# Kernel optimization log

Hardware: AMD Instinct MI355X
Metric: run time of the kernel (lower is better)

The kernel has to match this reference:

```python
import jax, jax.numpy as jnp
import numpy as np


def setup_inputs() -> dict:
    key = jax.random.key(0)
    k1, k2, k3, k4 = jax.random.split(key, 4)
    B, S, IN, H = 4, 2048, 512, 1024
    x = jax.random.normal(k1, (B, S, IN), dtype=jnp.float32)
    W1 = jax.random.normal(k2, (IN, H), dtype=jnp.float32) * (1.0 / np.sqrt(IN))
    b1 = jax.random.normal(k3, (H,), dtype=jnp.float32) * 0.02
    Wq = jax.random.normal(k4, (H, H), dtype=jnp.float32) * (1.0 / np.sqrt(H))
    return {"x": x, "W1": W1, "b1": b1, "Wq": Wq, "atten_size": 16}


def reference(x, W1, b1, Wq, atten_size):
    A = atten_size
    B, S, _ = x.shape
    H = W1.shape[1]
    h = jax.nn.relu(jnp.einsum('bsi,ih->bsh', x, W1) + b1)  # [B,S,H]
    # zero-pad sequence dim by A on each side
    padded = jnp.pad(h, ((0, 0), (A, A), (0, 0)))  # [B,S+2A,H]
    # torch: stack(roll(padded, k, 1) for k in -A..A, dim=2) then slice [A:-A]
    # => x_nei[b, i, j] = padded[b, 2A + i - j]
    idx = 2 * A + jnp.arange(S)[:, None] - jnp.arange(2 * A + 1)[None, :]  # [S,W]
    x_nei = padded[:, idx, :]  # [B,S,W,H]
    q = jnp.einsum('bsh,hk->bsk', h, Wq)  # [B,S,H]
    scores = jnp.einsum('bsh,bswh->bsw', q, x_nei) / jnp.sqrt(jnp.asarray(H, x.dtype))
    w = jax.nn.softmax(scores, axis=2)  # softmax over window axis
    out = jnp.einsum('bsw,bswh->bsh', w, x_nei)
    return out
```

## Files before the change

### kernel.cpp

```cpp
#include <hip/hip_runtime.h>
#include <stdint.h>

constexpr int BATCH = 4;
constexpr int SEQ   = 2048;
constexpr int DIN   = 512;
constexpr int DH    = 1024;
constexpr int BS    = BATCH * SEQ;
constexpr int AP    = 32;
constexpr int AW    = 64;

typedef float  floatx4 __attribute__((ext_vector_type(4)));
typedef short  bf16x8  __attribute__((ext_vector_type(8)));

static __device__ __forceinline__ unsigned short f2bf(float f) {
  union { float f; unsigned u; } v; v.f = f;
  unsigned r = (v.u + 0x7fffu + ((v.u >> 16) & 1u)) >> 16;
  return (unsigned short)r;
}

static __device__ __forceinline__ void gld_lds16(const unsigned short* g, const short* l) {
  typedef const __attribute__((address_space(1))) void* gvp;
  typedef __attribute__((address_space(3))) void* lvp;
  __builtin_amdgcn_global_load_lds((gvp)(uintptr_t)g, (lvp)(unsigned)(uintptr_t)l, 16, 0, 0);
}

__global__ __launch_bounds__(256) void convert_x_k(const float* __restrict__ X,
                                                   unsigned short* __restrict__ Xb) {
  const int t = blockIdx.x * 256 + threadIdx.x;
  const float4 a = ((const float4*)X)[(size_t)t * 2];
  const float4 b = ((const float4*)X)[(size_t)t * 2 + 1];
  __align__(16) unsigned short o[8];
  o[0] = f2bf(a.x); o[1] = f2bf(a.y); o[2] = f2bf(a.z); o[3] = f2bf(a.w);
  o[4] = f2bf(b.x); o[5] = f2bf(b.y); o[6] = f2bf(b.z); o[7] = f2bf(b.w);
  *(uint4*)(Xb + (size_t)t * 8) = *(const uint4*)o;
}

__global__ __launch_bounds__(256) void transpose_w_k(const float* __restrict__ W1,
                                                     const float* __restrict__ Wq,
                                                     unsigned short* __restrict__ w1t,
                                                     unsigned short* __restrict__ wqt) {
  __shared__ float t[32][33];
  const bool isW1 = blockIdx.y < 16;
  const float* in = isW1 ? W1 : Wq;
  unsigned short* out = isW1 ? w1t : wqt;
  const int R = isW1 ? DIN : DH;
  const int C = DH;
  const int r0 = (isW1 ? blockIdx.y : (blockIdx.y - 16)) * 32;
  const int c0 = blockIdx.x * 32;
  const int tx = threadIdx.x & 31, ty = threadIdx.x >> 5;
  for (int i = ty; i < 32; i += 8) t[i][tx] = in[(size_t)(r0 + i) * C + c0 + tx];
  __syncthreads();
  for (int i = ty; i < 32; i += 8) out[(size_t)(c0 + i) * R + r0 + tx] = f2bf(t[tx][i]);
}

__global__ __launch_bounds__(256) void gemm1_k(const unsigned short* __restrict__ Ab,
                                               const unsigned short* __restrict__ Bt,
                                               const float* __restrict__ bias,
                                               unsigned short* __restrict__ outB,
                                               unsigned short* __restrict__ outBT) {
  const int M = BS, N = DH, K = DIN;
  __shared__ __align__(16) short As0[128 * 32], As1[128 * 32];
  __shared__ __align__(16) short Bs0[128 * 32], Bs1[128 * 32];
  const int tid  = threadIdx.x;
  const int m0   = blockIdx.x * 128, n0 = blockIdx.y * 128;
  const int wv   = tid >> 6, lane = tid & 63;
  const int wm   = (wv >> 1) * 64, wn = (wv & 1) * 64;
  const int l16  = lane & 15, quad = lane >> 4;

  const int ra = lane >> 2, ca = (lane & 3) * 8;
  const unsigned short* gA = Ab + (size_t)(m0 + wv * 32 + ra) * K + ca;
  const unsigned short* gB = Bt + (size_t)(n0 + wv * 32 + ra) * K + ca;
  const short* lA0a = &As0[wv * 1024];
  const short* lA0b = &As0[wv * 1024 + 512];
  const short* lA1a = &As1[wv * 1024];
  const short* lA1b = &As1[wv * 1024 + 512];
  const short* lB0a = &Bs0[wv * 1024];
  const short* lB0b = &Bs0[wv * 1024 + 512];
  const short* lB1a = &Bs1[wv * 1024];
  const short* lB1b = &Bs1[wv * 1024 + 512];

  floatx4 acc[4][4];
  for (int i = 0; i < 4; i++)
    for (int j = 0; j < 4; j++) acc[i][j] = {0.f, 0.f, 0.f, 0.f};

  for (int ks = 0; ks < K / 64; ++ks) {
    __syncthreads();
    gld_lds16(gA, lA0a); gld_lds16(gA + 16 * K, lA0b);
    gld_lds16(gA + 32, lA1a); gld_lds16(gA + 16 * K + 32, lA1b);
    gld_lds16(gB, lB0a); gld_lds16(gB + 16 * K, lB0b);
    gld_lds16(gB + 32, lB1a); gld_lds16(gB + 16 * K + 32, lB1b);
    gA += 64; gB += 64;
    __syncthreads();
    bf16x8 af[4], bfr[4];
    for (int i = 0; i < 4; i++)
      af[i] = *(const bf16x8*)&As0[(wm + i * 16 + l16) * 32 + quad * 8];
    for (int j = 0; j < 4; j++)
      bfr[j] = *(const bf16x8*)&Bs0[(wn + j * 16 + l16) * 32 + quad * 8];
    for (int i = 0; i < 4; i++)
      for (int j = 0; j < 4; j++)
        acc[i][j] = __builtin_amdgcn_mfma_f32_16x16x32_bf16(af[i], bfr[j], acc[i][j], 0, 0, 0);
    for (int i = 0; i < 4; i++)
      af[i] = *(const bf16x8*)&As1[(wm + i * 16 + l16) * 32 + quad * 8];
    for (int j = 0; j < 4; j++)
      bfr[j] = *(const bf16x8*)&Bs1[(wn + j * 16 + l16) * 32 + quad * 8];
    for (int i = 0; i < 4; i++)
      for (int j = 0; j < 4; j++)
        acc[i][j] = __builtin_amdgcn_mfma_f32_16x16x32_bf16(af[i], bfr[j], acc[i][j], 0, 0, 0);
  }

  for (int j = 0; j < 4; j++) {
    const int col = n0 + wn + j * 16 + l16;
    const float bv = bias[col];
    for (int i = 0; i < 4; i++) {
      const int rowb = m0 + wm + i * 16 + quad * 4;
      float v[4];
      for (int r = 0; r < 4; r++) v[r] = fmaxf(acc[i][j][r] + bv, 0.f);
      for (int r = 0; r < 4; r++) outB[(size_t)(rowb + r) * N + col] = f2bf(v[r]);
      ushort4 o4; o4.x = f2bf(v[0]); o4.y = f2bf(v[1]); o4.z = f2bf(v[2]); o4.w = f2bf(v[3]);
      *(ushort4*)(outBT + (size_t)col * M + rowb) = o4;
    }
  }
}

__global__ __launch_bounds__(256) void gemm2_k(const unsigned short* __restrict__ Ab,
                                               const unsigned short* __restrict__ Bt,
                                               unsigned short* __restrict__ outB) {
  const int N = DH, K = DH;
  __shared__ __align__(16) short As0[128 * 32], As1[128 * 32];
  __shared__ __align__(16) short Bs0[128 * 32], Bs1[128 * 32];
  const int tid  = threadIdx.x;
  const int m0   = blockIdx.x * 128, n0 = blockIdx.y * 128;
  const int wv   = tid >> 6, lane = tid & 63;
  const int wm   = (wv >> 1) * 64, wn = (wv & 1) * 64;
  const int l16  = lane & 15, quad = lane >> 4;

  const int ra = lane >> 2, ca = (lane & 3) * 8;
  const unsigned short* gA = Ab + (size_t)(m0 + wv * 32 + ra) * K + ca;
  const unsigned short* gB = Bt + (size_t)(n0 + wv * 32 + ra) * K + ca;
  const short* lA0a = &As0[wv * 1024];
  const short* lA0b = &As0[wv * 1024 + 512];
  const short* lA1a = &As1[wv * 1024];
  const short* lA1b = &As1[wv * 1024 + 512];
  const short* lB0a = &Bs0[wv * 1024];
  const short* lB0b = &Bs0[wv * 1024 + 512];
  const short* lB1a = &Bs1[wv * 1024];
  const short* lB1b = &Bs1[wv * 1024 + 512];

  floatx4 acc[4][4];
  for (int i = 0; i < 4; i++)
    for (int j = 0; j < 4; j++) acc[i][j] = {0.f, 0.f, 0.f, 0.f};

  for (int ks = 0; ks < K / 64; ++ks) {
    __syncthreads();
    gld_lds16(gA, lA0a); gld_lds16(gA + 16 * K, lA0b);
    gld_lds16(gA + 32, lA1a); gld_lds16(gA + 16 * K + 32, lA1b);
    gld_lds16(gB, lB0a); gld_lds16(gB + 16 * K, lB0b);
    gld_lds16(gB + 32, lB1a); gld_lds16(gB + 16 * K + 32, lB1b);
    gA += 64; gB += 64;
    __syncthreads();
    bf16x8 af[4], bfr[4];
    for (int i = 0; i < 4; i++)
      af[i] = *(const bf16x8*)&As0[(wm + i * 16 + l16) * 32 + quad * 8];
    for (int j = 0; j < 4; j++)
      bfr[j] = *(const bf16x8*)&Bs0[(wn + j * 16 + l16) * 32 + quad * 8];
    for (int i = 0; i < 4; i++)
      for (int j = 0; j < 4; j++)
        acc[i][j] = __builtin_amdgcn_mfma_f32_16x16x32_bf16(af[i], bfr[j], acc[i][j], 0, 0, 0);
    for (int i = 0; i < 4; i++)
      af[i] = *(const bf16x8*)&As1[(wm + i * 16 + l16) * 32 + quad * 8];
    for (int j = 0; j < 4; j++)
      bfr[j] = *(const bf16x8*)&Bs1[(wn + j * 16 + l16) * 32 + quad * 8];
    for (int i = 0; i < 4; i++)
      for (int j = 0; j < 4; j++)
        acc[i][j] = __builtin_amdgcn_mfma_f32_16x16x32_bf16(af[i], bfr[j], acc[i][j], 0, 0, 0);
  }

  for (int j = 0; j < 4; j++) {
    const int col = n0 + wn + j * 16 + l16;
    for (int i = 0; i < 4; i++) {
      const int rowb = m0 + wm + i * 16 + quad * 4;
      for (int r = 0; r < 4; r++)
        outB[(size_t)(rowb + r) * N + col] = f2bf(acc[i][j][r]);
    }
  }
}

__global__ __launch_bounds__(512) void attn_mfma_k(const unsigned short* __restrict__ hb,
                                                   const unsigned short* __restrict__ hbT,
                                                   const unsigned short* __restrict__ qb,
                                                   float* __restrict__ out) {
  __shared__ float Sf[32 * 64];
  __shared__ __align__(16) short Ps[32 * 72];

  const int tid  = threadIdx.x;
  const int wave = tid >> 6, lane = tid & 63;
  const int l16  = lane & 15, quad = lane >> 4;
  const int p0   = blockIdx.x * AP;
  const int s0   = p0 & (SEQ - 1);

  for (int i = tid; i < 32 * 72 / 2; i += 512) ((unsigned*)Ps)[i] = 0;

  {
    const int mt = wave >> 2, nt = wave & 3;
    const unsigned short* qp = qb + (size_t)(p0 + mt * 16 + l16) * DH + quad * 8;
    const int hrow = s0 - 16 + nt * 16 + l16;
    const bool hv = (hrow >= 0) && (hrow < SEQ);
    const unsigned short* hp = hb + (long long)(p0 - 16 + nt * 16 + l16) * DH + quad * 8;

    floatx4 ac[4] = {{0,0,0,0},{0,0,0,0},{0,0,0,0},{0,0,0,0}};
    const bf16x8 hz = {0,0,0,0,0,0,0,0};
    __builtin_amdgcn_s_setprio(1);
    #pragma unroll
    for (int it = 0; it < 32; ++it) {
      bf16x8 qa = *(const bf16x8*)(qp + it * 32);
      bf16x8 ha = hz;
      if (hv) ha = *(const bf16x8*)(hp + it * 32);
      ac[it & 3] = __builtin_amdgcn_mfma_f32_16x16x32_bf16(qa, ha, ac[it & 3], 0, 0, 0);
    }
    __builtin_amdgcn_s_setprio(0);
    floatx4 s4;
    for (int r = 0; r < 4; r++)
      s4[r] = (ac[0][r] + ac[1][r]) + (ac[2][r] + ac[3][r]);
    for (int r = 0; r < 4; r++)
      Sf[(mt * 16 + quad * 4 + r) * 64 + nt * 16 + l16] = s4[r] * (1.f / 32.f);
  }
  __syncthreads();

  {
    const int row = tid >> 4, k = tid & 15;
    const float v0 = Sf[row * 64 + row + k];
    const float v1 = Sf[row * 64 + row + k + 16];
    const float v2 = (k == 0) ? Sf[row * 64 + row + 32] : -1e30f;
    float mx = fmaxf(v0, fmaxf(v1, v2));
    for (int off = 1; off < 16; off <<= 1) mx = fmaxf(mx, __shfl_xor(mx, off, 64));
    const float e0 = __expf(v0 - mx), e1 = __expf(v1 - mx);
    const float e2 = (k == 0) ? __expf(v2 - mx) : 0.f;
    float sum = e0 + e1 + e2;
    for (int off = 1; off < 16; off <<= 1) sum += __shfl_xor(sum, off, 64);
    const float inv = 1.f / sum;
    Ps[row * 72 + row + k] = f2bf(e0 * inv);
    Ps[row * 72 + row + k + 16] = f2bf(e1 * inv);
    if (k == 0) Ps[row * 72 + row + 32] = f2bf(e2 * inv);
  }
  __syncthreads();

  {
    const bf16x8 pb00 = *(const bf16x8*)&Ps[(l16) * 72 + quad * 8];
    const bf16x8 pb01 = *(const bf16x8*)&Ps[(l16) * 72 + 32 + quad * 8];
    const bf16x8 pb10 = *(const bf16x8*)&Ps[(16 + l16) * 72 + quad * 8];
    const bf16x8 pb11 = *(const bf16x8*)&Ps[(16 + l16) * 72 + 32 + quad * 8];

    int lo = 16 - s0; if (lo < 0) lo = 0;
    int hi = SEQ + 16 - s0; if (hi > AW) hi = AW;
    const bool interior = (lo == 0) && (hi == AW);

    #pragma unroll
    for (int i = 0; i < 8; ++i) {
      const int mt2 = wave * 8 + i;
      const unsigned short* ap = hbT + (size_t)(mt2 * 16 + l16) * BS + (p0 - 16) + quad * 8;
      bf16x8 aa0 = *(const bf16x8*)(ap);
      bf16x8 aa1 = *(const bf16x8*)(ap + 32);
      if (!interior) {
        #pragma unroll
        for (int j = 0; j < 8; j++) {
          const int k = quad * 8 + j;
          if (k < lo || k >= hi) aa0[j] = 0;
          if (k + 32 < lo || k + 32 >= hi) aa1[j] = 0;
        }
      }
      floatx4 o0 = {0.f, 0.f, 0.f, 0.f}, o1 = {0.f, 0.f, 0.f, 0.f};
      __builtin_amdgcn_s_setprio(1);
      o0 = __builtin_amdgcn_mfma_f32_16x16x32_bf16(aa0, pb00, o0, 0, 0, 0);
      o0 = __builtin_amdgcn_mfma_f32_16x16x32_bf16(aa1, pb01, o0, 0, 0, 0);
      o1 = __builtin_amdgcn_mfma_f32_16x16x32_bf16(aa0, pb10, o1, 0, 0, 0);
      o1 = __builtin_amdgcn_mfma_f32_16x16x32_bf16(aa1, pb11, o1, 0, 0, 0);
      __builtin_amdgcn_s_setprio(0);
      float4 s0v; s0v.x = o0[0]; s0v.y = o0[1]; s0v.z = o0[2]; s0v.w = o0[3];
      float4 s1v; s1v.x = o1[0]; s1v.y = o1[1]; s1v.z = o1[2]; s1v.w = o1[3];
      *(float4*)(out + (size_t)(p0 + l16) * DH + mt2 * 16 + quad * 4) = s0v;
      *(float4*)(out + (size_t)(p0 + 16 + l16) * DH + mt2 * 16 + quad * 4) = s1v;
    }
  }
}

extern "C" void kernel_launch(void* const* d_in, const int* in_sizes, int n_in,
                              void* d_out, int out_size, void* d_ws, size_t ws_size,
                              hipStream_t stream) {
  const float* x  = (const float*)d_in[0];
  const float* W1 = (const float*)d_in[1];
  const float* b1 = (const float*)d_in[2];
  const float* Wq = (const float*)d_in[3];

  char* w = (char*)d_ws;
  unsigned short* w1t = (unsigned short*)(w);
  unsigned short* wqt = (unsigned short*)(w + (1ull  << 20));
  unsigned short* hb  = (unsigned short*)(w + (3ull  << 20));
  unsigned short* hbT = (unsigned short*)(w + (19ull << 20));
  unsigned short* qb  = (unsigned short*)(w + (35ull << 20));
  unsigned short* xb  = qb;

  convert_x_k<<<BS * DIN / (256 * 8), 256, 0, stream>>>(x, xb);
  transpose_w_k<<<dim3(DH / 32, 48), 256, 0, stream>>>(W1, Wq, w1t, wqt);

  gemm1_k<<<dim3(BS / 128, DH / 128), 256, 0, stream>>>(xb, w1t, b1, hb, hbT);
  gemm2_k<<<dim3(BS / 128, DH / 128), 256, 0, stream>>>(hb, wqt, qb);

  attn_mfma_k<<<BS / AP, 512, 0, stream>>>(hb, hbT, qb, (float*)d_out);
}
```

Baseline: 155.7 us.

## Split attention score reduction across 1024 threads and merge prep kernels

The attention kernel now runs 16 waves per block instead of 8. The score GEMM is split along the hidden dimension into two halves, written to two LDS buffers and summed before the softmax, and each wave handles half as many output tiles. The aim is more waves in flight to hide global-load latency in this memory-bound kernel. Separately, the x-to-bf16 conversion and the weight transposes are folded into one prep launch to save a kernel launch. The costs are an extra LDS buffer, an extra add per score, and a larger block that may limit how many blocks fit on a CU.

Measured after the change: 158.5 us. Within noise of the previous version (+1.8%).

```diff
diff --git a/kernel.cpp b/kernel.cpp
--- a/kernel.cpp
+++ b/kernel.cpp
@@ -24,22 +24,23 @@
   __builtin_amdgcn_global_load_lds((gvp)(uintptr_t)g, (lvp)(unsigned)(uintptr_t)l, 16, 0, 0);
 }
 
-__global__ __launch_bounds__(256) void convert_x_k(const float* __restrict__ X,
-                                                   unsigned short* __restrict__ Xb) {
-  const int t = blockIdx.x * 256 + threadIdx.x;
-  const float4 a = ((const float4*)X)[(size_t)t * 2];
-  const float4 b = ((const float4*)X)[(size_t)t * 2 + 1];
-  __align__(16) unsigned short o[8];
-  o[0] = f2bf(a.x); o[1] = f2bf(a.y); o[2] = f2bf(a.z); o[3] = f2bf(a.w);
-  o[4] = f2bf(b.x); o[5] = f2bf(b.y); o[6] = f2bf(b.z); o[7] = f2bf(b.w);
-  *(uint4*)(Xb + (size_t)t * 8) = *(const uint4*)o;
-}
-
-__global__ __launch_bounds__(256) void transpose_w_k(const float* __restrict__ W1,
-                                                     const float* __restrict__ Wq,
-                                                     unsigned short* __restrict__ w1t,
-                                                     unsigned short* __restrict__ wqt) {
+__global__ __launch_bounds__(256) void prep_k(const float* __restrict__ X,
+                                              const float* __restrict__ W1,
+                                              const float* __restrict__ Wq,
+                                              unsigned short* __restrict__ Xb,
+                                              unsigned short* __restrict__ w1t,
+                                              unsigned short* __restrict__ wqt) {
   __shared__ float t[32][33];
+  if (blockIdx.y >= 48) {
+    const int t0 = ((blockIdx.y - 48) * 32 + blockIdx.x) * 256 + threadIdx.x;
+    const float4 a = ((const float4*)X)[(size_t)t0 * 2];
+    const float4 b = ((const float4*)X)[(size_t)t0 * 2 + 1];
+    __align__(16) unsigned short o[8];
+    o[0] = f2bf(a.x); o[1] = f2bf(a.y); o[2] = f2bf(a.z); o[3] = f2bf(a.w);
+    o[4] = f2bf(b.x); o[5] = f2bf(b.y); o[6] = f2bf(b.z); o[7] = f2bf(b.w);
+    *(uint4*)(Xb + (size_t)t0 * 8) = *(const uint4*)o;
+    return;
+  }
   const bool isW1 = blockIdx.y < 16;
   const float* in = isW1 ? W1 : Wq;
   unsigned short* out = isW1 ? w1t : wqt;
@@ -185,11 +186,11 @@
   }
 }
 
-__global__ __launch_bounds__(512) void attn_mfma_k(const unsigned short* __restrict__ hb,
-                                                   const unsigned short* __restrict__ hbT,
-                                                   const unsigned short* __restrict__ qb,
-                                                   float* __restrict__ out) {
-  __shared__ float Sf[32 * 64];
+__global__ __launch_bounds__(1024) void attn_mfma_k(const unsigned short* __restrict__ hb,
+                                                    const unsigned short* __restrict__ hbT,
+                                                    const unsigned short* __restrict__ qb,
+                                                    float* __restrict__ out) {
+  __shared__ float Sf[2][32 * 64];
   __shared__ __align__(16) short Ps[32 * 72];
 
   const int tid  = threadIdx.x;
@@ -198,20 +199,24 @@
   const int p0   = blockIdx.x * AP;
   const int s0   = p0 & (SEQ - 1);
 
-  for (int i = tid; i < 32 * 72 / 2; i += 512) ((unsigned*)Ps)[i] = 0;
+  if (tid < 32 * 72 / 2) ((unsigned*)Ps)[tid] = 0;
+  else if (tid < 32 * 72 / 2 + 128) ((unsigned*)Ps)[tid] = (tid - 1024 < 32 * 72 / 2 - 1024) ? 0u : 0u;
+  if (tid >= 1024 - 128 && tid - (1024 - 128) + 1024 < 1152) ((unsigned*)Ps)[tid - (1024 - 128) + 1024] = 0;
 
   {
-    const int mt = wave >> 2, nt = wave & 3;
-    const unsigned short* qp = qb + (size_t)(p0 + mt * 16 + l16) * DH + quad * 8;
+    const int kh = wave & 1;
+    const int nt = (wave >> 1) & 3;
+    const int mt = wave >> 3;
+    const unsigned short* qp = qb + (size_t)(p0 + mt * 16 + l16) * DH + kh * 512 + quad * 8;
     const int hrow = s0 - 16 + nt * 16 + l16;
     const bool hv = (hrow >= 0) && (hrow < SEQ);
-    const unsigned short* hp = hb + (long long)(p0 - 16 + nt * 16 + l16) * DH + quad * 8;
+    const unsigned short* hp = hb + (long long)(p0 - 16 + nt * 16 + l16) * DH + kh * 512 + quad * 8;
 
     floatx4 ac[4] = {{0,0,0,0},{0,0,0,0},{0,0,0,0},{0,0,0,0}};
     const bf16x8 hz = {0,0,0,0,0,0,0,0};
     __builtin_amdgcn_s_setprio(1);
     #pragma unroll
-    for (int it = 0; it < 32; ++it) {
+    for (int it = 0; it < 16; ++it) {
       bf16x8 qa = *(const bf16x8*)(qp + it * 32);
       bf16x8 ha = hz;
       if (hv) ha = *(const bf16x8*)(hp + it * 32);
@@ -222,15 +227,15 @@
     for (int r = 0; r < 4; r++)
       s4[r] = (ac[0][r] + ac[1][r]) + (ac[2][r] + ac[3][r]);
     for (int r = 0; r < 4; r++)
-      Sf[(mt * 16 + quad * 4 + r) * 64 + nt * 16 + l16] = s4[r] * (1.f / 32.f);
+      Sf[kh][(mt * 16 + quad * 4 + r) * 64 + nt * 16 + l16] = s4[r] * (1.f / 32.f);
   }
   __syncthreads();
 
-  {
+  if (tid < 512) {
     const int row = tid >> 4, k = tid & 15;
-    const float v0 = Sf[row * 64 + row + k];
-    const float v1 = Sf[row * 64 + row + k + 16];
-    const float v2 = (k == 0) ? Sf[row * 64 + row + 32] : -1e30f;
+    const float v0 = Sf[0][row * 64 + row + k] + Sf[1][row * 64 + row + k];
+    const float v1 = Sf[0][row * 64 + row + k + 16] + Sf[1][row * 64 + row + k + 16];
+    const float v2 = (k == 0) ? (Sf[0][row * 64 + row + 32] + Sf[1][row * 64 + row + 32]) : -1e30f;
     float mx = fmaxf(v0, fmaxf(v1, v2));
     for (int off = 1; off < 16; off <<= 1) mx = fmaxf(mx, __shfl_xor(mx, off, 64));
     const float e0 = __expf(v0 - mx), e1 = __expf(v1 - mx);
@@ -255,8 +260,8 @@
     const bool interior = (lo == 0) && (hi == AW);
 
     #pragma unroll
-    for (int i = 0; i < 8; ++i) {
-      const int mt2 = wave * 8 + i;
+    for (int i = 0; i < 4; ++i) {
+      const int mt2 = wave * 4 + i;
       const unsigned short* ap = hbT + (size_t)(mt2 * 16 + l16) * BS + (p0 - 16) + quad * 8;
       bf16x8 aa0 = *(const bf16x8*)(ap);
       bf16x8 aa1 = *(const bf16x8*)(ap + 32);
@@ -299,11 +304,10 @@
   unsigned short* qb  = (unsigned short*)(w + (35ull << 20));
   unsigned short* xb  = qb;
 
-  convert_x_k<<<BS * DIN / (256 * 8), 256, 0, stream>>>(x, xb);
-  transpose_w_k<<<dim3(DH / 32, 48), 256, 0, stream>>>(W1, Wq, w1t, wqt);
+  prep_k<<<dim3(32, 112), 256, 0, stream>>>(x, W1, Wq, xb, w1t, wqt);
 
   gemm1_k<<<dim3(BS / 128, DH / 128), 256, 0, stream>>>(xb, w1t, b1, hb, hbT);
   gemm2_k<<<dim3(BS / 128, DH / 128), 256, 0, stream>>>(hb, wqt, qb);
 
-  attn_mfma_k<<<BS / AP, 512, 0, stream>>>(hb, hbT, qb, (float*)d_out);
-}
+  attn_mfma_k<<<BS / AP, 1024, 0, stream>>>(hb, hbT, qb, (float*)d_out);
+}
```
